# Kernel optimization log

Hardware: AMD Instinct MI355X
Metric: run time of the kernel (lower is better)

## Reference

```python
import jax, jax.numpy as jnp
import numpy as np

N, KLEN, Q, S, E, H = 8, 512, 16, 128, 256, 8


def setup_inputs() -> dict:
    key = jax.random.key(0)
    ks = jax.random.split(key, 9)
    values = jax.random.normal(ks[0], (N, KLEN, E), dtype=jnp.float32)
    keys = jax.random.normal(ks[1], (N, KLEN, E), dtype=jnp.float32)
    query = jax.random.normal(ks[2], (N, Q, S, E), dtype=jnp.float32)
    mask = jax.random.randint(ks[3], (N, 1, 1, KLEN, 1), 0, 2, dtype=jnp.int32)
    Wv = jax.random.normal(ks[4], (E, E), dtype=jnp.float32) * 0.02
    Wk = jax.random.normal(ks[5], (E, E), dtype=jnp.float32) * 0.02
    Wq = jax.random.normal(ks[6], (E, E), dtype=jnp.float32) * 0.02
    Wo = jax.random.normal(ks[7], (E, H * E), dtype=jnp.float32) * 0.02
    bo = jnp.zeros((E,), dtype=jnp.float32)
    return {"values": values, "keys": keys, "query": query, "mask": mask,
            "Wv": Wv, "Wk": Wk, "Wq": Wq, "Wo": Wo, "bo": bo}


def reference(values, keys, query, mask, Wv, Wk, Wq, Wo, bo):
    # In the torch module head_dim == embed_size and the SAME Linear is applied
    # to every (expanded) head, so project once and broadcast over heads.
    e = Wq.shape[0]
    heads = Wo.shape[1] // e
    v = values @ Wv.T          # [N, K, E]
    k = keys @ Wk.T            # [N, K, E]
    q = query @ Wq.T           # [N, Q, S, E]
    # energy per head is identical; broadcast to [N, H, Q, K, S] to mirror
    # torch's einsum('nqshd,nkhd->nhqks') followed by masked_fill.
    energy = jnp.einsum('nqsd,nkd->nqks', q, k)               # [N, Q, K, S]
    energy = jnp.broadcast_to(energy[:, None],
                              (energy.shape[0], heads) + energy.shape[1:])
    energy = jnp.where(mask == 0, jnp.float32(-1e20), energy)  # [N,H,Q,K,S]
    attn = jax.nn.softmax(energy / jnp.sqrt(jnp.float32(e)), axis=3)
    out = jnp.einsum('nhqks,nkd->nqshd', attn, v)              # [N,Q,S,H,E]
    out = out.reshape(out.shape[0], out.shape[1], out.shape[2], heads * e)
    return out @ Wo.T + bo                                     # [N, Q, S, E]
```

## Files before the change

### kernel.cpp

```cpp
#include <hip/hip_runtime.h>
#include <hip/hip_bf16.h>
#include <stdint.h>

#define NB   8
#define KL   512
#define QD   16
#define SD   128
#define ED   256
#define RPN  (QD*SD)
#define BMR  32
#define FRAG 512
#define PAN  131072

typedef __hip_bfloat16 bf16;
using s16x8 = __attribute__((ext_vector_type(8))) short;
using f32x4 = __attribute__((ext_vector_type(4))) float;

__device__ __forceinline__ float b2f(unsigned short u){
    union { uint32_t i; float f; } v; v.i = ((uint32_t)u) << 16; return v.f;
}
__device__ __forceinline__ unsigned short f2b(float f){
    union { float ff; uint32_t i; } v; v.ff = f;
    uint32_t lsb = (v.i >> 16) & 1;
    v.i += 0x7FFFu + lsb;
    return (unsigned short)(v.i >> 16);
}
__device__ __forceinline__ uint32_t cvtpk(float lo, float hi){
    uint32_t r;
    asm("v_cvt_pk_bf16_f32 %0, %1, %2" : "=v"(r) : "v"(lo), "v"(hi));
    return r;
}
__device__ __forceinline__ f32x4 mfma16(s16x8 a, s16x8 b, f32x4 c){
    return __builtin_amdgcn_mfma_f32_16x16x32_bf16(a, b, c, 0, 0, 0);
}

template<bool B>
__device__ __forceinline__ float ldin(const void* p, size_t i){
    if (B) return b2f(((const unsigned short*)p)[i]);
    else   return ((const float*)p)[i];
}

__device__ bool probe_bf16(const uint32_t* __restrict__ w, int* pc){
    if (threadIdx.x == 0) *pc = 0;
    __syncthreads();
    if (threadIdx.x < 256){
        int local = 0;
        #pragma unroll
        for (int i = 0; i < 4; ++i){
            uint32_t x = w[threadIdx.x*4 + i];
            uint32_t e = (x >> 7) & 0xFFu;
            local += (e >= 120u && e <= 132u) ? 1 : 0;
        }
        if (local) atomicAdd(pc, local);
    }
    __syncthreads();
    return *pc > 512;
}

template<bool B>
__device__ void gt_body(const void* __restrict__ Wq, const void* __restrict__ Wk,
                        float* __restrict__ Gt, int bx){
    int b = bx, a = threadIdx.x;
    float s = 0.f;
    #pragma unroll 8
    for (int d = 0; d < 256; ++d)
        s += ldin<B>(Wq, (size_t)d*256 + a) * ldin<B>(Wk, (size_t)d*256 + b);
    Gt[b*256 + a] = s;
}
template<bool B>
__device__ void wosmt_body(const void* __restrict__ Wo, const void* __restrict__ Wv,
                           float* __restrict__ Mt, int bx, float (*sm)[256]){
    int t = threadIdx.x, e0 = bx*8;
    #pragma unroll
    for (int je = 0; je < 8; ++je){
        int e = e0 + je;
        float s = 0.f;
        #pragma unroll
        for (int h = 0; h < 8; ++h) s += ldin<B>(Wo, (size_t)e*2048 + h*256 + t);
        sm[je][t] = s;
    }
    __syncthreads();
    float acc[8] = {0,0,0,0,0,0,0,0};
    #pragma unroll 4
    for (int dp = 0; dp < 256; ++dp){
        float wv = ldin<B>(Wv, (size_t)dp*256 + t);
        #pragma unroll
        for (int je = 0; je < 8; ++je) acc[je] += sm[je][dp] * wv;
    }
    #pragma unroll
    for (int je = 0; je < 8; ++je) Mt[t*256 + e0 + je] = acc[je];
}
__global__ __launch_bounds__(256)
void k_prep(const void* __restrict__ values,
            const void* __restrict__ Wq, const void* __restrict__ Wk,
            const void* __restrict__ Wo, const void* __restrict__ Wv,
            float* __restrict__ Gt, float* __restrict__ Mt){
    __shared__ float sm[8][256];
    __shared__ int pc;
    bool bf = probe_bf16((const uint32_t*)values, &pc);
    if (blockIdx.x < 256){
        if (bf) gt_body<true >(Wq, Wk, Gt, blockIdx.x);
        else    gt_body<false>(Wq, Wk, Gt, blockIdx.x);
    } else {
        int bx = blockIdx.x - 256;
        if (bf) wosmt_body<true >(Wo, Wv, Mt, bx, sm);
        else    wosmt_body<false>(Wo, Wv, Mt, bx, sm);
    }
}

template<bool B>
__device__ void projK_body(const void* __restrict__ A, const float* __restrict__ Wt,
                           unsigned short* __restrict__ C, int bx, float (*As)[256]){
    int r0 = bx * 8;
    int t  = threadIdx.x;
    #pragma unroll
    for (int j = 0; j < 8; ++j)
        As[j][t] = ldin<B>(A, (size_t)(r0 + j)*256 + t);
    __syncthreads();
    float acc[8] = {0,0,0,0,0,0,0,0};
    #pragma unroll 4
    for (int i = 0; i < 256; ++i){
        float w = Wt[i*256 + t];
        #pragma unroll
        for (int j = 0; j < 8; ++j) acc[j] += As[j][i] * w;
    }
    int nn = r0 >> 9, key0 = r0 & 511;
    int K16 = key0 >> 4, ks = t >> 5, g = (t >> 3) & 3, i = t & 7;
    size_t base = (size_t)nn*PAN + (size_t)((K16*8 + ks)*64)*8;
    int l0 = (key0 & 15) | (g << 4);
    #pragma unroll
    for (int j = 0; j < 8; ++j)
        C[base + (size_t)(l0 + j)*8 + i] = f2b(acc[j]);
}
template<bool B>
__device__ void projU_body(const void* __restrict__ A, const float* __restrict__ Wt,
                           unsigned short* __restrict__ C, int bx, float (*As)[256]){
    int r0 = bx * 8;
    int t  = threadIdx.x;
    #pragma unroll
    for (int j = 0; j < 8; ++j)
        As[j][t] = ldin<B>(A, (size_t)(r0 + j)*256 + t);
    __syncthreads();
    float acc[8] = {0,0,0,0,0,0,0,0};
    #pragma unroll 4
    for (int i = 0; i < 256; ++i){
        float w = Wt[i*256 + t];
        #pragma unroll
        for (int j = 0; j < 8; ++j) acc[j] += As[j][i] * w;
    }
    int nn = r0 >> 9, k0 = r0 & 511;
    int ks2 = k0 >> 5, g = (k0 >> 3) & 3;
    int E16 = t >> 4, l = (t & 15) | (g << 4);
    size_t base = (size_t)nn*PAN + (size_t)((E16*16 + ks2)*64 + l)*8;
    union { s16x8 v; unsigned short h[8]; } pk;
    #pragma unroll
    for (int j = 0; j < 8; ++j) pk.h[j] = f2b(acc[j]);
    *(s16x8*)(&C[base]) = pk.v;
}
__global__ __launch_bounds__(256)
void k_proj2(const void* __restrict__ keys, const void* __restrict__ values,
             const float* __restrict__ Gt, const float* __restrict__ Mt,
             unsigned short* __restrict__ kkF, unsigned short* __restrict__ utF){
    __shared__ float As[8][256];
    __shared__ int pc;
    bool bf = probe_bf16((const uint32_t*)values, &pc);
    if (blockIdx.x < 512){
        if (bf) projK_body<true >(keys, Gt, kkF, blockIdx.x, As);
        else    projK_body<false>(keys, Gt, kkF, blockIdx.x, As);
    } else {
        int bx = blockIdx.x - 512;
        if (bf) projU_body<true >(values, Mt, utF, bx, As);
        else    projU_body<false>(values, Mt, utF, bx, As);
    }
}

template<bool B>
__device__ void fused_body(const void* __restrict__ query,
                           const unsigned short* __restrict__ kkF,
                           const unsigned short* __restrict__ utF,
                           const int* __restrict__ mask,
                           const void* __restrict__ bo,
                           void* __restrict__ out,
                           unsigned short* Qs, unsigned short* Pf,
                           float* redM, float* redS){
    int bid = blockIdx.x;
    int n   = bid & 7;
    int r0  = (bid >> 3) * BMR;
    int t   = threadIdx.x;
    int l15 = t & 15;
    int g   = (t >> 4) & 3;
    int w   = t >> 6;
    int lane = t & 63;

    const unsigned short* Kn = kkF + (size_t)n*PAN;
    const unsigned short* Un = utF + (size_t)n*PAN;
    const int* mn = mask + n*KL;

    {
        int row = t >> 4;
        int c0  = (t & 15) * 16;
        int sw  = (row & 7) << 3;
        size_t qoff = (size_t)n*RPN*ED + (size_t)(r0 + row)*ED + c0;
        if (B){
            const unsigned short* qp = (const unsigned short*)query + qoff;
            s16x8 v0 = *(const s16x8*)(qp);
            s16x8 v1 = *(const s16x8*)(qp + 8);
            *(s16x8*)&Qs[(row*ED + c0    ) ^ sw] = v0;
            *(s16x8*)&Qs[(row*ED + c0 + 8) ^ sw] = v1;
        } else {
            const float* qp = (const float*)query + qoff;
            float4 x0 = *(const float4*)(qp);
            float4 x1 = *(const float4*)(qp + 4);
            float4 x2 = *(const float4*)(qp + 8);
            float4 x3 = *(const float4*)(qp + 12);
            union { s16x8 v; uint32_t u[4]; } pk;
            pk.u[0] = cvtpk(x0.x,x0.y); pk.u[1] = cvtpk(x0.z,x0.w);
            pk.u[2] = cvtpk(x1.x,x1.y); pk.u[3] = cvtpk(x1.z,x1.w);
            *(s16x8*)&Qs[(row*ED + c0    ) ^ sw] = pk.v;
            pk.u[0] = cvtpk(x2.x,x2.y); pk.u[1] = cvtpk(x2.z,x2.w);
            pk.u[2] = cvtpk(x3.x,x3.y); pk.u[3] = cvtpk(x3.z,x3.w);
            *(s16x8*)&Qs[(row*ED + c0 + 8) ^ sw] = pk.v;
        }
    }
    __syncthreads();

    int asw = (l15 & 7) << 3;

    float p[2][4][4];
    {
        f32x4 acc1[2][4];
        #pragma unroll
        for (int rt = 0; rt < 2; ++rt)
            #pragma unroll
            for (int c = 0; c < 4; ++c) acc1[rt][c] = (f32x4){0.f,0.f,0.f,0.f};

        const unsigned short* kb = Kn + (size_t)w*16384 + (size_t)lane*8;
        s16x8 bb[3][4];
        auto LDK = [&](int KS, int SL){
            #pragma unroll
            for (int c = 0; c < 4; ++c)
                bb[SL][c] = *(const s16x8*)(kb + (size_t)(c*8 + KS)*FRAG);
        };
        LDK(0,0); LDK(1,1);
        #pragma unroll
        for (int ks = 0; ks < 8; ++ks){
            if (ks + 2 < 8) LDK(ks + 2, (ks + 2) % 3);
            int col = ks*32 + g*8;
            s16x8 a0 = *(const s16x8*)&Qs[(( 0 + l15)*ED + col) ^ asw];
            s16x8 a1 = *(const s16x8*)&Qs[((16 + l15)*ED + col) ^ asw];
            #pragma unroll
            for (int c = 0; c < 4; ++c){
                acc1[0][c] = mfma16(a0, bb[ks % 3][c], acc1[0][c]);
                acc1[1][c] = mfma16(a1, bb[ks % 3][c], acc1[1][c]);
            }
        }
        #pragma unroll
        for (int c = 0; c < 4; ++c){
            bool zz = (mn[w*64 + c*16 + l15] == 0);
            #pragma unroll
            for (int rt = 0; rt < 2; ++rt)
                #pragma unroll
                for (int j = 0; j < 4; ++j)
                    p[rt][c][j] = zz ? -1e20f : acc1[rt][c][j] * 0.0625f;
        }
    }

    {
        float mx[2][4];
        #pragma unroll
        for (int rt = 0; rt < 2; ++rt)
            #pragma unroll
            for (int j = 0; j < 4; ++j){
                float m0 = fmaxf(fmaxf(p[rt][0][j], p[rt][1][j]),
                                 fmaxf(p[rt][2][j], p[rt][3][j]));
                #pragma unroll
                for (int off = 1; off < 16; off <<= 1)
                    m0 = fmaxf(m0, __shfl_xor(m0, off, 16));
                mx[rt][j] = m0;
            }
        if (l15 == 0){
            #pragma unroll
            for (int rt = 0; rt < 2; ++rt)
                #pragma unroll
                for (int j = 0; j < 4; ++j)
                    redM[(rt*16 + g*4 + j)*8 + w] = mx[rt][j];
        }
        __syncthreads();
        float sm[2][4];
        #pragma unroll
        for (int rt = 0; rt < 2; ++rt)
            #pragma unroll
            for (int j = 0; j < 4; ++j){
                int row = rt*16 + g*4 + j;
                float4 a = *(const float4*)&redM[row*8];
                float4 b = *(const float4*)&redM[row*8 + 4];
                float m = fmaxf(fmaxf(fmaxf(a.x,a.y),fmaxf(a.z,a.w)),
                                fmaxf(fmaxf(b.x,b.y),fmaxf(b.z,b.w)));
                float s = 0.f;
                #pragma unroll
                for (int c = 0; c < 4; ++c){
                    p[rt][c][j] = __expf(p[rt][c][j] - m);
                    s += p[rt][c][j];
                }
                #pragma unroll
                for (int off = 1; off < 16; off <<= 1)
                    s += __shfl_xor(s, off, 16);
                sm[rt][j] = s;
            }
        if (l15 == 0){
            #pragma unroll
            for (int rt = 0; rt < 2; ++rt)
                #pragma unroll
                for (int j = 0; j < 4; ++j)
                    redS[(rt*16 + g*4 + j)*8 + w] = sm[rt][j];
        }
        __syncthreads();
        int ihi = ((l15 >> 3) << 4);
        int ilo = l15 & 7;
        #pragma unroll
        for (int rt = 0; rt < 2; ++rt){
            #pragma unroll
            for (int j = 0; j < 4; ++j){
                int row = rt*16 + g*4 + j;
                float4 a = *(const float4*)&redS[row*8];
                float4 b = *(const float4*)&redS[row*8 + 4];
                float inv = 1.0f / ((a.x+a.y+a.z+a.w) + (b.x+b.y+b.z+b.w));
                #pragma unroll
                for (int c = 0; c < 4; ++c){
                    int lp = (g*4 + j) | (((c & 1) << 5) | ihi);
                    int elem = (rt*16 + w*2 + (c >> 1))*FRAG + lp*8 + ilo;
                    Pf[elem] = f2b(p[rt][c][j] * inv);
                }
            }
        }
    }
    __syncthreads();

    {
        f32x4 acc2[2][2];
        #pragma unroll
        for (int rt = 0; rt < 2; ++rt)
            #pragma unroll
            for (int c = 0; c < 2; ++c) acc2[rt][c] = (f32x4){0.f,0.f,0.f,0.f};

        const unsigned short* ub = Un + (size_t)(2*w)*8192 + (size_t)lane*8;
        s16x8 bu[3][2];
        auto LDU = [&](int KS, int SL){
            #pragma unroll
            for (int c = 0; c < 2; ++c)
                bu[SL][c] = *(const s16x8*)(ub + (size_t)(c*16 + KS)*FRAG);
        };
        LDU(0,0); LDU(1,1);
        #pragma unroll
        for (int ks = 0; ks < 16; ++ks){
            if (ks + 2 < 16) LDU(ks + 2, (ks + 2) % 3);
            s16x8 p0 = *(const s16x8*)&Pf[( 0 + ks)*FRAG + lane*8];
            s16x8 p1 = *(const s16x8*)&Pf[(16 + ks)*FRAG + lane*8];
            #pragma unroll
            for (int c = 0; c < 2; ++c){
                acc2[0][c] = mfma16(p0, bu[ks % 3][c], acc2[0][c]);
                acc2[1][c] = mfma16(p1, bu[ks % 3][c], acc2[1][c]);
            }
        }
        float bov[2];
        #pragma unroll
        for (int c = 0; c < 2; ++c) bov[c] = ldin<B>(bo, (2*w + c)*16 + l15);
        #pragma unroll
        for (int rt = 0; rt < 2; ++rt){
            #pragma unroll
            for (int j = 0; j < 4; ++j){
                int row = rt*16 + g*4 + j;
                #pragma unroll
                for (int c = 0; c < 2; ++c){
                    int e = (2*w + c)*16 + l15;
                    float val = acc2[rt][c][j] + bov[c];
                    size_t oidx = (size_t)n*RPN*ED + (size_t)(r0 + row)*ED + e;
                    if (B) ((unsigned short*)out)[oidx] = f2b(val);
                    else   ((float*)out)[oidx] = val;
                }
            }
        }
    }
}

__global__ __launch_bounds__(512, 4)
void k_fused4(const void* __restrict__ values, const void* __restrict__ query,
              const unsigned short* __restrict__ kkF,
              const unsigned short* __restrict__ utF,
              const int* __restrict__ mask, const void* __restrict__ bo,
              void* __restrict__ out){
    __shared__ unsigned short Qs[BMR*ED];
    __shared__ unsigned short Pf[32*FRAG];
    __shared__ float redM[BMR*8];
    __shared__ float redS[BMR*8];
    __shared__ int pc;
    bool bf = probe_bf16((const uint32_t*)values, &pc);
    if (bf) fused_body<true >(query, kkF, utF, mask, bo, out, Qs, Pf, redM, redS);
    else    fused_body<false>(query, kkF, utF, mask, bo, out, Qs, Pf, redM, redS);
}

extern "C" void kernel_launch(void* const* d_in, const int* in_sizes, int n_in,
                              void* d_out, int out_size, void* d_ws, size_t ws_size,
                              hipStream_t stream){
    const void* values = d_in[0];
    const void* keys   = d_in[1];
    const void* query  = d_in[2];
    const int*  mask   = (const int*)d_in[3];
    const void* Wv     = d_in[4];
    const void* Wk     = d_in[5];
    const void* Wq     = d_in[6];
    const void* Wo     = d_in[7];
    const void* bo     = d_in[8];

    float* ws = (float*)d_ws;
    float* ws_gt = ws;
    float* ws_mt = ws + 65536;
    unsigned short* ws_kk = (unsigned short*)(ws + 131072);
    unsigned short* ws_u  = ws_kk + (size_t)NB*PAN;

    k_prep  <<< 288, 256, 0, stream>>>(values, Wq, Wk, Wo, Wv, ws_gt, ws_mt);
    k_proj2 <<<1024, 256, 0, stream>>>(keys, values, ws_gt, ws_mt, ws_kk, ws_u);
    k_fused4<<< 512, 512, 0, stream>>>(values, query, ws_kk, ws_u, mask, bo, d_out);
}
```

Measured before the change: 152.8 us.

## Move key/value projection to split-bf16 MFMA with pre-swizzled weight fragments

The prep kernel now writes the combined weight matrices as high/low bf16 pairs in an MFMA fragment layout, not as fp32 row-major. The projection kernel drops its scalar fp32 FMA loop for 16x16x32 bf16 MFMA. It uses a three-term split-precision product to stay near fp32 accuracy, and stages results through LDS so they are written out with vector stores in the fragment layout the fused kernel expects. This is meant to cut the cost of the projection stage, which was a CUDA-core GEMM, at the price of extra MFMAs for the precision split and some rounding error.

```diff
diff --git a/kernel.cpp b/kernel.cpp
--- a/kernel.cpp
+++ b/kernel.cpp
@@ -19,6 +19,12 @@
 __device__ __forceinline__ float b2f(unsigned short u){
     union { uint32_t i; float f; } v; v.i = ((uint32_t)u) << 16; return v.f;
 }
+__device__ __forceinline__ float b2f_hi(uint32_t u){
+    union { uint32_t i; float f; } v; v.i = u & 0xFFFF0000u; return v.f;
+}
+__device__ __forceinline__ float b2f_lo(uint32_t u){
+    union { uint32_t i; float f; } v; v.i = u << 16; return v.f;
+}
 __device__ __forceinline__ unsigned short f2b(float f){
     union { float ff; uint32_t i; } v; v.ff = f;
     uint32_t lsb = (v.i >> 16) & 1;
@@ -57,19 +63,28 @@
     return *pc > 512;
 }
 
+__device__ __forceinline__ int waddr(int i, int o){
+    return (((o >> 4)*8 + (i >> 5)) << 9) + (((o & 15) | (((i >> 3) & 3) << 4)) << 3) + (i & 7);
+}
+
 template<bool B>
 __device__ void gt_body(const void* __restrict__ Wq, const void* __restrict__ Wk,
-                        float* __restrict__ Gt, int bx){
+                        unsigned short* __restrict__ WgH,
+                        unsigned short* __restrict__ WgL, int bx){
     int b = bx, a = threadIdx.x;
     float s = 0.f;
     #pragma unroll 8
     for (int d = 0; d < 256; ++d)
         s += ldin<B>(Wq, (size_t)d*256 + a) * ldin<B>(Wk, (size_t)d*256 + b);
-    Gt[b*256 + a] = s;
+    unsigned short hi = f2b(s);
+    unsigned short lo = f2b(s - b2f(hi));
+    int ad = waddr(b, a);
+    WgH[ad] = hi; WgL[ad] = lo;
 }
 template<bool B>
 __device__ void wosmt_body(const void* __restrict__ Wo, const void* __restrict__ Wv,
-                           float* __restrict__ Mt, int bx, float (*sm)[256]){
+                           unsigned short* __restrict__ WmH,
+                           unsigned short* __restrict__ WmL, int bx, float (*sm)[256]){
     int t = threadIdx.x, e0 = bx*8;
     #pragma unroll
     for (int je = 0; je < 8; ++je){
@@ -88,89 +103,141 @@
         for (int je = 0; je < 8; ++je) acc[je] += sm[je][dp] * wv;
     }
     #pragma unroll
-    for (int je = 0; je < 8; ++je) Mt[t*256 + e0 + je] = acc[je];
+    for (int je = 0; je < 8; ++je){
+        unsigned short hi = f2b(acc[je]);
+        unsigned short lo = f2b(acc[je] - b2f(hi));
+        int ad = waddr(t, e0 + je);
+        WmH[ad] = hi; WmL[ad] = lo;
+    }
 }
 __global__ __launch_bounds__(256)
 void k_prep(const void* __restrict__ values,
             const void* __restrict__ Wq, const void* __restrict__ Wk,
             const void* __restrict__ Wo, const void* __restrict__ Wv,
-            float* __restrict__ Gt, float* __restrict__ Mt){
+            unsigned short* __restrict__ WgH, unsigned short* __restrict__ WgL,
+            unsigned short* __restrict__ WmH, unsigned short* __restrict__ WmL){
     __shared__ float sm[8][256];
     __shared__ int pc;
     bool bf = probe_bf16((const uint32_t*)values, &pc);
     if (blockIdx.x < 256){
-        if (bf) gt_body<true >(Wq, Wk, Gt, blockIdx.x);
-        else    gt_body<false>(Wq, Wk, Gt, blockIdx.x);
+        if (bf) gt_body<true >(Wq, Wk, WgH, WgL, blockIdx.x);
+        else    gt_body<false>(Wq, Wk, WgH, WgL, blockIdx.x);
     } else {
         int bx = blockIdx.x - 256;
-        if (bf) wosmt_body<true >(Wo, Wv, Mt, bx, sm);
-        else    wosmt_body<false>(Wo, Wv, Mt, bx, sm);
+        if (bf) wosmt_body<true >(Wo, Wv, WmH, WmL, bx, sm);
+        else    wosmt_body<false>(Wo, Wv, WmH, WmL, bx, sm);
     }
 }
 
 template<bool B>
-__device__ void projK_body(const void* __restrict__ A, const float* __restrict__ Wt,
-                           unsigned short* __restrict__ C, int bx, float (*As)[256]){
-    int r0 = bx * 8;
-    int t  = threadIdx.x;
+__device__ void projM_body(const void* __restrict__ A,
+                           const unsigned short* __restrict__ WH,
+                           const unsigned short* __restrict__ WL,
+                           unsigned short* __restrict__ outF,
+                           int bx8, bool keysHalf, unsigned short* St){
+    int t = threadIdx.x, lane = t & 63, w = t >> 6;
+    int l15 = t & 15, g = (t >> 4) & 3;
+    int r0 = bx8 * 16;
+
+    f32x4 acc[2];
+    acc[0] = (f32x4){0.f,0.f,0.f,0.f};
+    acc[1] = (f32x4){0.f,0.f,0.f,0.f};
+
+    s16x8 wh[3][2], wl[3][2];
+    auto LDW = [&](int ks, int sl){
+        #pragma unroll
+        for (int c = 0; c < 2; ++c){
+            size_t off = (size_t)(((w*2 + c)*8 + ks)*512 + lane*8);
+            wh[sl][c] = *(const s16x8*)(WH + off);
+            wl[sl][c] = *(const s16x8*)(WL + off);
+        }
+    };
+    float4 ar[2][2];
+    s16x8  ab[2];
+    auto LDA = [&](int ks, int sl){
+        size_t idx = (size_t)(r0 + l15)*256 + ks*32 + g*8;
+        if (B) ab[sl] = *(const s16x8*)((const unsigned short*)A + idx);
+        else { ar[sl][0] = *(const float4*)((const float*)A + idx);
+               ar[sl][1] = *(const float4*)((const float*)A + idx + 4); }
+    };
+    LDW(0,0); LDW(1,1); LDA(0,0); LDA(1,1);
+
     #pragma unroll
-    for (int j = 0; j < 8; ++j)
-        As[j][t] = ldin<B>(A, (size_t)(r0 + j)*256 + t);
-    __syncthreads();
-    float acc[8] = {0,0,0,0,0,0,0,0};
-    #pragma unroll 4
-    for (int i = 0; i < 256; ++i){
-        float w = Wt[i*256 + t];
-        #pragma unroll
-        for (int j = 0; j < 8; ++j) acc[j] += As[j][i] * w;
-    }
-    int nn = r0 >> 9, key0 = r0 & 511;
-    int K16 = key0 >> 4, ks = t >> 5, g = (t >> 3) & 3, i = t & 7;
-    size_t base = (size_t)nn*PAN + (size_t)((K16*8 + ks)*64)*8;
-    int l0 = (key0 & 15) | (g << 4);
+    for (int ks = 0; ks < 8; ++ks){
+        int s = ks & 1, sw = ks % 3;
+        s16x8 ah, al;
+        if (B){
+            ah = ab[s];
+        } else {
+            union { s16x8 v; uint32_t u[4]; } H, L;
+            float4 x0 = ar[s][0], x1 = ar[s][1];
+            H.u[0] = cvtpk(x0.x, x0.y); H.u[1] = cvtpk(x0.z, x0.w);
+            H.u[2] = cvtpk(x1.x, x1.y); H.u[3] = cvtpk(x1.z, x1.w);
+            L.u[0] = cvtpk(x0.x - b2f_lo(H.u[0]), x0.y - b2f_hi(H.u[0]));
+            L.u[1] = cvtpk(x0.z - b2f_lo(H.u[1]), x0.w - b2f_hi(H.u[1]));
+            L.u[2] = cvtpk(x1.x - b2f_lo(H.u[2]), x1.y - b2f_hi(H.u[2]));
+            L.u[3] = cvtpk(x1.z - b2f_lo(H.u[3]), x1.w - b2f_hi(H.u[3]));
+            ah = H.v; al = L.v;
+        }
+        if (ks + 2 < 8) LDA(ks + 2, s);
+        #pragma unroll
+        for (int c = 0; c < 2; ++c){
+            acc[c] = mfma16(ah, wh[sw][c], acc[c]);
+            if (!B) acc[c] = mfma16(al, wh[sw][c], acc[c]);
+            acc[c] = mfma16(ah, wl[sw][c], acc[c]);
+        }
+        if (ks + 2 < 8) LDW(ks + 2, (ks + 2) % 3);
+    }
+
+    int n   = bx8 >> 5;
+    int r0n = r0 & 511;
     #pragma unroll
-    for (int j = 0; j < 8; ++j)
-        C[base + (size_t)(l0 + j)*8 + i] = f2b(acc[j]);
-}
-template<bool B>
-__device__ void projU_body(const void* __restrict__ A, const float* __restrict__ Wt,
-                           unsigned short* __restrict__ C, int bx, float (*As)[256]){
-    int r0 = bx * 8;
-    int t  = threadIdx.x;
-    #pragma unroll
-    for (int j = 0; j < 8; ++j)
-        As[j][t] = ldin<B>(A, (size_t)(r0 + j)*256 + t);
-    __syncthreads();
-    float acc[8] = {0,0,0,0,0,0,0,0};
-    #pragma unroll 4
-    for (int i = 0; i < 256; ++i){
-        float w = Wt[i*256 + t];
-        #pragma unroll
-        for (int j = 0; j < 8; ++j) acc[j] += As[j][i] * w;
-    }
-    int nn = r0 >> 9, k0 = r0 & 511;
-    int ks2 = k0 >> 5, g = (k0 >> 3) & 3;
-    int E16 = t >> 4, l = (t & 15) | (g << 4);
-    size_t base = (size_t)nn*PAN + (size_t)((E16*16 + ks2)*64 + l)*8;
-    union { s16x8 v; unsigned short h[8]; } pk;
-    #pragma unroll
-    for (int j = 0; j < 8; ++j) pk.h[j] = f2b(acc[j]);
-    *(s16x8*)(&C[base]) = pk.v;
-}
-__global__ __launch_bounds__(256)
-void k_proj2(const void* __restrict__ keys, const void* __restrict__ values,
-             const float* __restrict__ Gt, const float* __restrict__ Mt,
+    for (int c = 0; c < 2; ++c){
+        #pragma unroll
+        for (int j = 0; j < 4; ++j){
+            int row = g*4 + j;
+            int col = (w*2 + c)*16 + l15;
+            int idx;
+            if (keysHalf)
+                idx = ((col >> 5) << 9) + (((row & 15) | (((col >> 3) & 3) << 4)) << 3) + (col & 7);
+            else {
+                int key = r0n + row;
+                idx = ((col >> 4) << 8) + ((((col & 15) | (((key >> 3) & 1) << 4))) << 3) + (key & 7);
+            }
+            St[idx] = f2b(acc[c][j]);
+        }
+    }
+    __syncthreads();
+
+    int s8 = t * 8;
+    if (keysHalf){
+        size_t base = (size_t)n*PAN + (size_t)((r0n >> 4) * 8) * 512;
+        *(s16x8*)(outF + base + s8) = *(const s16x8*)(St + s8);
+    } else {
+        int ks2 = r0n >> 5;
+        int fl = s8 >> 8, off = s8 & 255;
+        int halfbase = ((r0n >> 4) & 1) * 256;
+        *(s16x8*)(outF + (size_t)n*PAN + (size_t)((fl*16 + ks2)*512 + halfbase + off))
+            = *(const s16x8*)(St + s8);
+    }
+}
+__global__ __launch_bounds__(512)
+void k_projM(const void* __restrict__ keys, const void* __restrict__ values,
+             const unsigned short* __restrict__ WgH, const unsigned short* __restrict__ WgL,
+             const unsigned short* __restrict__ WmH, const unsigned short* __restrict__ WmL,
              unsigned short* __restrict__ kkF, unsigned short* __restrict__ utF){
-    __shared__ float As[8][256];
+    __shared__ unsigned short St[4096];
     __shared__ int pc;
     bool bf = probe_bf16((const uint32_t*)values, &pc);
-    if (blockIdx.x < 512){
-        if (bf) projK_body<true >(keys, Gt, kkF, blockIdx.x, As);
-        else    projK_body<false>(keys, Gt, kkF, blockIdx.x, As);
+    int bx = blockIdx.x;
+    bool keysHalf = (bx < 256);
+    int bx8 = bx & 255;
+    if (keysHalf){
+        if (bf) projM_body<true >(keys, WgH, WgL, kkF, bx8, true, St);
+        else    projM_body<false>(keys, WgH, WgL, kkF, bx8, true, St);
     } else {
-        int bx = blockIdx.x - 512;
-        if (bf) projU_body<true >(values, Mt, utF, bx, As);
-        else    projU_body<false>(values, Mt, utF, bx, As);
+        if (bf) projM_body<true >(values, WmH, WmL, utF, bx8, false, St);
+        else    projM_body<false>(values, WmH, WmL, utF, bx8, false, St);
     }
 }
 
@@ -412,13 +479,15 @@
     const void* Wo     = d_in[7];
     const void* bo     = d_in[8];
 
-    float* ws = (float*)d_ws;
-    float* ws_gt = ws;
-    float* ws_mt = ws + 65536;
-    unsigned short* ws_kk = (unsigned short*)(ws + 131072);
+    unsigned short* wsu = (unsigned short*)d_ws;
+    unsigned short* wgh = wsu;
+    unsigned short* wgl = wsu + 65536;
+    unsigned short* wmh = wsu + 131072;
+    unsigned short* wml = wsu + 196608;
+    unsigned short* ws_kk = wsu + 262144;
     unsigned short* ws_u  = ws_kk + (size_t)NB*PAN;
 
-    k_prep  <<< 288, 256, 0, stream>>>(values, Wq, Wk, Wo, Wv, ws_gt, ws_mt);
-    k_proj2 <<<1024, 256, 0, stream>>>(keys, values, ws_gt, ws_mt, ws_kk, ws_u);
+    k_prep  <<< 288, 256, 0, stream>>>(values, Wq, Wk, Wo, Wv, wgh, wgl, wmh, wml);
+    k_projM <<< 512, 512, 0, stream>>>(keys, values, wgh, wgl, wmh, wml, ws_kk, ws_u);
     k_fused4<<< 512, 512, 0, stream>>>(values, query, ws_kk, ws_u, mask, bo, d_out);
 }
```

New measurement: 142.7 us. 1.07x faster.
